# Kernel optimization log

Measured on AMD Instinct MI355X. Metric: run time of the kernel, lower is better.

## Reference

```python
import jax, jax.numpy as jnp
import numpy as np

GN_EPS = 1e-5
G = 8          # SKA groups
SKS3 = 27      # sks**3


def _aff(x, s, b):
    # folded BatchNorm (eval): per-channel scale + shift on NCDHW tensor
    return x * s[None, :, None, None, None] + b[None, :, None, None, None]


def _c1(x, w):
    # 1x1x1 conv as channel GEMM; w: [O, I]
    return jnp.einsum('bcdhw,oc->bodhw', x, w)


def _dw5(x, w):
    # depthwise 5x5x5 conv, pad=2; w: [C, 1, 5, 5, 5]
    return jax.lax.conv_general_dilated(
        x, w, window_strides=(1, 1, 1), padding=[(2, 2)] * 3,
        dimension_numbers=('NCDHW', 'OIDHW', 'NCDHW'),
        feature_group_count=x.shape[1])


def setup_inputs() -> dict:
    key = jax.random.key(0)
    ks = jax.random.split(key, 24)
    B, C, D, H, W = 2, 64, 32, 32, 32

    def n(k, shape, scale=1.0):
        return jax.random.normal(k, shape, jnp.float32) * scale

    def u(k, shape):
        return jax.random.uniform(k, shape, jnp.float32, 0.5, 1.5)

    return {
        'x': n(ks[0], (B, C, D, H, W)),
        'w1': n(ks[1], (32, 64), 64 ** -0.5),
        's1': u(ks[2], (32,)), 'b1': n(ks[3], (32,), 0.1),
        'w2': n(ks[4], (32, 1, 5, 5, 5), 125 ** -0.5),
        's2': u(ks[5], (32,)), 'b2': n(ks[6], (32,), 0.1),
        'w3': n(ks[7], (32, 32), 32 ** -0.5),
        's3': u(ks[8], (32,)), 'b3': n(ks[9], (32,), 0.1),
        'w4': n(ks[10], (216, 32), 32 ** -0.5), 'b4': n(ks[11], (216,), 0.1),
        'gn_g': u(ks[12], (216,)), 'gn_b': n(ks[13], (216,), 0.1),
        'bn_s': u(ks[14], (64,)), 'bn_b': n(ks[15], (64,), 0.1),
        'pw1_w': n(ks[16], (128, 64), 64 ** -0.5),
        'pw1_s': u(ks[17], (128,)), 'pw1_b': n(ks[18], (128,), 0.1),
        'pw2_w': n(ks[19], (64, 128), 128 ** -0.5),
        'pw2_s': u(ks[20], (64,)), 'pw2_b': n(ks[21], (64,), 0.1),
    }


def reference(x, w1, s1, b1, w2, s2, b2, w3, s3, b3, w4, b4,
              gn_g, gn_b, bn_s, bn_b,
              pw1_w, pw1_s, pw1_b, pw2_w, pw2_s, pw2_b):
    B, C, D, H, W = x.shape

    # ---- LKP3D: dynamic kernel generation ----
    a = jax.nn.relu(_aff(_c1(x, w1), s1, b1))          # cv1 + BN + ReLU
    a = _aff(_dw5(a, w2), s2, b2)                      # cv2 (5^3 dw) + BN
    a = jax.nn.relu(_aff(_c1(a, w3), s3, b3))          # cv3 + BN + ReLU
    wk = _c1(a, w4) + b4[None, :, None, None, None]    # cv4: [B,216,D,H,W]
    # GroupNorm: num_groups = dim//groups = 8, channels = 216
    g = wk.reshape(B, G, SKS3, D, H, W)
    mu = g.mean(axis=(2, 3, 4, 5), keepdims=True)
    var = g.var(axis=(2, 3, 4, 5), keepdims=True)
    g = (g - mu) * jax.lax.rsqrt(var + GN_EPS)
    wk = g.reshape(B, G * SKS3, D, H, W) * gn_g[None, :, None, None, None] \
         + gn_b[None, :, None, None, None]
    wk = wk.reshape(B, G, SKS3, D, H, W)               # [B, G, 27, D, H, W]

    # ---- SKA3D: apply dynamic kernels (27 shifted copies, grouped) ----
    offs = [(di, hi, wi) for di in (-1, 0, 1) for hi in (-1, 0, 1) for wi in (-1, 0, 1)]
    patches = jnp.stack(
        [jnp.roll(x, (-di, -hi, -wi), axis=(2, 3, 4)) for di, hi, wi in offs],
        axis=2)                                        # [B, C, 27, D, H, W]
    p = patches.reshape(B, G, C // G, SKS3, D, H, W)
    sk = jnp.einsum('bgckdhw,bgkdhw->bgcdhw', p, wk).reshape(B, C, D, H, W)

    y = _aff(sk, bn_s, bn_b) + x                       # LSConv BN + residual

    # ---- FFN (residual): pw1 + BN + ReLU + pw2 + BN ----
    f = jax.nn.relu(_aff(_c1(y, pw1_w), pw1_s, pw1_b))
    f = _aff(_c1(f, pw2_w), pw2_s, pw2_b)
    return y + f
```

## Files before the change

### kernel.cpp

```cpp
#include <hip/hip_runtime.h>
#include <hip/hip_bf16.h>

#define SPAT 32768
#define BATCH 2
#define GN_EPS 1e-5f

__device__ __forceinline__ void fma4(float4& a, const float4& v, float w) {
    a.x = fmaf(v.x, w, a.x); a.y = fmaf(v.y, w, a.y);
    a.z = fmaf(v.z, w, a.z); a.w = fmaf(v.w, w, a.w);
}

template <bool RELU, bool AFF>
__global__ __launch_bounds__(256) void k_c1(
    const float* __restrict__ in, const float* __restrict__ w,
    const float* __restrict__ sc, const float* __restrict__ bi,
    float* __restrict__ out, int Cin, int Cout)
{
    int q = blockIdx.x * 256 + threadIdx.x;
    int s = q * 4;
    int o0 = blockIdx.y * 4, b = blockIdx.z;
    const float* ip = in + (size_t)b * Cin * SPAT + s;
    float4 a0 = {0,0,0,0}, a1 = a0, a2 = a0, a3 = a0;
#pragma unroll 4
    for (int c = 0; c < Cin; ++c) {
        float4 v = *(const float4*)(ip + (size_t)c * SPAT);
        fma4(a0, v, w[(o0+0)*Cin + c]);
        fma4(a1, v, w[(o0+1)*Cin + c]);
        fma4(a2, v, w[(o0+2)*Cin + c]);
        fma4(a3, v, w[(o0+3)*Cin + c]);
    }
    float4 accs[4] = {a0, a1, a2, a3};
#pragma unroll
    for (int i = 0; i < 4; ++i) {
        int o = o0 + i;
        float scale = AFF ? sc[o] : 1.f;
        float shift = bi[o];
        float4 r = accs[i];
        r.x = r.x * scale + shift; r.y = r.y * scale + shift;
        r.z = r.z * scale + shift; r.w = r.w * scale + shift;
        if (RELU) {
            r.x = fmaxf(r.x, 0.f); r.y = fmaxf(r.y, 0.f);
            r.z = fmaxf(r.z, 0.f); r.w = fmaxf(r.w, 0.f);
        }
        *(float4*)(out + ((size_t)b * Cout + o) * SPAT + s) = r;
    }
}

__global__ __launch_bounds__(256) void k_cv4(
    const float* __restrict__ in, const float* __restrict__ w,
    const float* __restrict__ bi, float* __restrict__ out,
    float* __restrict__ partial)
{
    int q = blockIdx.x * 256 + threadIdx.x;
    int s = q * 4;
    int o0 = blockIdx.y * 4, b = blockIdx.z;
    const float* ip = in + (size_t)b * 32 * SPAT + s;
    float4 a0 = {0,0,0,0}, a1 = a0, a2 = a0, a3 = a0;
#pragma unroll 4
    for (int c = 0; c < 32; ++c) {
        float4 v = *(const float4*)(ip + (size_t)c * SPAT);
        fma4(a0, v, w[(o0+0)*32 + c]);
        fma4(a1, v, w[(o0+1)*32 + c]);
        fma4(a2, v, w[(o0+2)*32 + c]);
        fma4(a3, v, w[(o0+3)*32 + c]);
    }
    float4 accs[4] = {a0, a1, a2, a3};
    float sums[4], sss[4];
#pragma unroll
    for (int i = 0; i < 4; ++i) {
        int o = o0 + i;
        float shift = bi[o];
        float4 r = accs[i];
        r.x += shift; r.y += shift; r.z += shift; r.w += shift;
        *(float4*)(out + ((size_t)b * 216 + o) * SPAT + s) = r;
        sums[i] = r.x + r.y + r.z + r.w;
        sss[i]  = r.x*r.x + r.y*r.y + r.z*r.z + r.w*r.w;
    }
#pragma unroll
    for (int off = 32; off > 0; off >>= 1) {
#pragma unroll
        for (int i = 0; i < 4; ++i) {
            sums[i] += __shfl_down(sums[i], off, 64);
            sss[i]  += __shfl_down(sss[i],  off, 64);
        }
    }
    __shared__ float sh[4][4][2];
    int wave = threadIdx.x >> 6, lane = threadIdx.x & 63;
    if (lane == 0) {
#pragma unroll
        for (int i = 0; i < 4; ++i) {
            sh[wave][i][0] = sums[i];
            sh[wave][i][1] = sss[i];
        }
    }
    __syncthreads();
    if (threadIdx.x < 4) {
        int i = threadIdx.x;
        float s0 = sh[0][i][0] + sh[1][i][0] + sh[2][i][0] + sh[3][i][0];
        float s1 = sh[0][i][1] + sh[1][i][1] + sh[2][i][1] + sh[3][i][1];
        int o = o0 + i;
        int idx = (((b * 216 + o) * 32) + blockIdx.x) * 2;
        partial[idx + 0] = s0;
        partial[idx + 1] = s1;
    }
}

__global__ __launch_bounds__(256) void k_gn_stats2(
    const float* __restrict__ partial, float* __restrict__ stats)
{
    int bg = blockIdx.x;
    int b = bg >> 3, g = bg & 7;
    float sum = 0.f, ss = 0.f;
    for (int i = threadIdx.x; i < 27 * 32; i += 256) {
        int o = g * 27 + (i >> 5);
        int xb = i & 31;
        int idx = ((b * 216 + o) * 32 + xb) * 2;
        sum += partial[idx + 0];
        ss  += partial[idx + 1];
    }
    __shared__ float sh[512];
    sh[threadIdx.x] = sum; sh[256 + threadIdx.x] = ss;
    __syncthreads();
    for (int off = 128; off > 0; off >>= 1) {
        if (threadIdx.x < off) {
            sh[threadIdx.x] += sh[threadIdx.x + off];
            sh[256 + threadIdx.x] += sh[256 + threadIdx.x + off];
        }
        __syncthreads();
    }
    if (threadIdx.x == 0) {
        stats[bg * 2 + 0] = sh[0];
        stats[bg * 2 + 1] = sh[256];
    }
}

__global__ __launch_bounds__(256) void k_ska(
    const float* __restrict__ x, const float* __restrict__ wk,
    const float* __restrict__ stats,
    const float* __restrict__ gn_g, const float* __restrict__ gn_b,
    const float* __restrict__ bn_s, const float* __restrict__ bn_b,
    float* __restrict__ y)
{
    int q = blockIdx.x * 256 + threadIdx.x;
    int s = q * 4;
    int g = blockIdx.y, b = blockIdx.z;
    int bg = b * 8 + g;
    const float N = 27.f * (float)SPAT;
    float mu  = stats[bg * 2 + 0] / N;
    float var = stats[bg * 2 + 1] / N - mu * mu;
    float inv = rsqrtf(var + GN_EPS);
    int d = s >> 10, h = (s >> 5) & 31, w0 = s & 31;
    int lane = threadIdx.x & 63;
    int xl_src = (lane & 56) | ((lane + 7) & 7);
    int xr_src = (lane & 56) | ((lane + 1) & 7);
    const float* xg = x + ((size_t)(b * 64 + g * 8)) * SPAT;
    const float* wp = wk + ((size_t)(b * 216 + g * 27)) * SPAT + s;

    float4 acc[8];
    float4 xc[8];
#pragma unroll
    for (int c = 0; c < 8; ++c) acc[c] = {0,0,0,0};

#pragma unroll
    for (int kd = 0; kd < 3; ++kd) {
        int zd = (d + kd + 31) & 31;
#pragma unroll
        for (int kh = 0; kh < 3; ++kh) {
            int zh = (h + kh + 31) & 31;
            int kbase = (kd * 3 + kh) * 3;
            float wn[3][4];
#pragma unroll
            for (int kw = 0; kw < 3; ++kw) {
                int kk = kbase + kw;
                float4 wq = *(const float4*)(wp + (size_t)kk * SPAT);
                float gg = gn_g[g * 27 + kk], gb = gn_b[g * 27 + kk];
                wn[kw][0] = (wq.x - mu) * inv * gg + gb;
                wn[kw][1] = (wq.y - mu) * inv * gg + gb;
                wn[kw][2] = (wq.z - mu) * inv * gg + gb;
                wn[kw][3] = (wq.w - mu) * inv * gg + gb;
            }
            int rowoff = zd * 1024 + zh * 32;
            bool center = (kd == 1) && (kh == 1);
#pragma unroll
            for (int c = 0; c < 8; ++c) {
                float4 m = *(const float4*)(xg + (size_t)c * SPAT + rowoff + w0);
                if (center) xc[c] = m;
                float xl = __shfl(m.w, xl_src, 64);
                float xr = __shfl(m.x, xr_src, 64);
                float win[6] = {xl, m.x, m.y, m.z, m.w, xr};
#pragma unroll
                for (int kw = 0; kw < 3; ++kw) {
                    acc[c].x = fmaf(win[0 + kw], wn[kw][0], acc[c].x);
                    acc[c].y = fmaf(win[1 + kw], wn[kw][1], acc[c].y);
                    acc[c].z = fmaf(win[2 + kw], wn[kw][2], acc[c].z);
                    acc[c].w = fmaf(win[3 + kw], wn[kw][3], acc[c].w);
                }
            }
        }
    }
#pragma unroll
    for (int c = 0; c < 8; ++c) {
        int ch = g * 8 + c;
        float bs = bn_s[ch], bb = bn_b[ch];
        float4 r;
        r.x = acc[c].x * bs + bb + xc[c].x;
        r.y = acc[c].y * bs + bb + xc[c].y;
        r.z = acc[c].z * bs + bb + xc[c].z;
        r.w = acc[c].w * bs + bb + xc[c].w;
        *(float4*)(y + ((size_t)(b * 64 + ch)) * SPAT + s) = r;
    }
}

__global__ __launch_bounds__(256) void k_dw5(
    const float* __restrict__ in, const float* __restrict__ w2,
    const float* __restrict__ s2, const float* __restrict__ b2,
    float* __restrict__ out)
{
    __shared__ float lds[8 * 36 * 40];
    int tid = threadIdx.x;
    int d0 = blockIdx.x * 4;
    int c = blockIdx.y, b = blockIdx.z;
    const float* ip = in + ((size_t)(b * 32 + c)) * SPAT;

    float4 z = {0,0,0,0};
    for (int i = tid; i < 8 * 36 * 40 / 4; i += 256)
        ((float4*)lds)[i] = z;
    __syncthreads();
    for (int i = tid; i < 8 * 256; i += 256) {
        int p = i >> 8, rem = i & 255;
        int r = rem >> 3, c4 = (rem & 7) * 4;
        int d = d0 - 2 + p;
        if (d >= 0 && d < 32) {
            float4 v = *(const float4*)(ip + d * 1024 + r * 32 + c4);
            *(float4*)&lds[p * 1440 + (r + 2) * 40 + (c4 + 4)] = v;
        }
    }
    __syncthreads();

    float scl = s2[c], shf = b2[c];
    const float* wt = w2 + c * 125;
#pragma unroll
    for (int k = 0; k < 4; ++k) {
        int j = tid + k * 256;
        int pd = j >> 8, rem = j & 255;
        int hr = rem >> 3, w4 = (rem & 7) * 4;
        float4 acc = {0,0,0,0};
#pragma unroll
        for (int kd = 0; kd < 5; ++kd) {
            const float* pl = &lds[(pd + kd) * 1440];
#pragma unroll
            for (int kh = 0; kh < 5; ++kh) {
                const float* row = pl + (hr + kh) * 40 + w4;
                float4 r0 = *(const float4*)(row);
                float4 r1 = *(const float4*)(row + 4);
                float4 r2 = *(const float4*)(row + 8);
                float win[12] = {r0.x, r0.y, r0.z, r0.w,
                                 r1.x, r1.y, r1.z, r1.w,
                                 r2.x, r2.y, r2.z, r2.w};
#pragma unroll
                for (int kw = 0; kw < 5; ++kw) {
                    float wv = wt[kd * 25 + kh * 5 + kw];
                    acc.x = fmaf(wv, win[2 + 0 + kw], acc.x);
                    acc.y = fmaf(wv, win[2 + 1 + kw], acc.y);
                    acc.z = fmaf(wv, win[2 + 2 + kw], acc.z);
                    acc.w = fmaf(wv, win[2 + 3 + kw], acc.w);
                }
            }
        }
        acc.x = acc.x * scl + shf; acc.y = acc.y * scl + shf;
        acc.z = acc.z * scl + shf; acc.w = acc.w * scl + shf;
        *(float4*)(out + ((size_t)(b * 32 + c)) * SPAT
                   + (d0 + pd) * 1024 + hr * 32 + w4) = acc;
    }
}

__global__ __launch_bounds__(256) void k_pw2_out(
    const float* __restrict__ f1, const float* __restrict__ w,
    const float* __restrict__ sc, const float* __restrict__ bi,
    const float* __restrict__ yres, float* __restrict__ out)
{
    int q = blockIdx.x * 256 + threadIdx.x;
    int s = q * 4;
    int o0 = blockIdx.y * 4, b = blockIdx.z;
    const float* ip = f1 + (size_t)b * 128 * SPAT + s;
    float4 a0 = {0,0,0,0}, a1 = a0, a2 = a0, a3 = a0;
#pragma unroll 4
    for (int c = 0; c < 128; ++c) {
        float4 v = *(const float4*)(ip + (size_t)c * SPAT);
        fma4(a0, v, w[(o0+0)*128 + c]);
        fma4(a1, v, w[(o0+1)*128 + c]);
        fma4(a2, v, w[(o0+2)*128 + c]);
        fma4(a3, v, w[(o0+3)*128 + c]);
    }
    float4 accs[4] = {a0, a1, a2, a3};
#pragma unroll
    for (int i = 0; i < 4; ++i) {
        int o = o0 + i;
        float scale = sc[o], shift = bi[o];
        float4 yv = *(const float4*)(yres + ((size_t)(b * 64 + o)) * SPAT + s);
        float4 r = accs[i];
        r.x = r.x * scale + shift + yv.x;
        r.y = r.y * scale + shift + yv.y;
        r.z = r.z * scale + shift + yv.z;
        r.w = r.w * scale + shift + yv.w;
        *(float4*)(out + ((size_t)(b * 64 + o)) * SPAT + s) = r;
    }
}

extern "C" void kernel_launch(void* const* d_in, const int* in_sizes, int n_in,
                              void* d_out, int out_size, void* d_ws, size_t ws_size,
                              hipStream_t stream)
{
    const float* x     = (const float*)d_in[0];
    const float* w1    = (const float*)d_in[1];
    const float* s1    = (const float*)d_in[2];
    const float* b1    = (const float*)d_in[3];
    const float* w2    = (const float*)d_in[4];
    const float* s2    = (const float*)d_in[5];
    const float* b2    = (const float*)d_in[6];
    const float* w3    = (const float*)d_in[7];
    const float* s3    = (const float*)d_in[8];
    const float* b3    = (const float*)d_in[9];
    const float* w4    = (const float*)d_in[10];
    const float* b4    = (const float*)d_in[11];
    const float* gn_g  = (const float*)d_in[12];
    const float* gn_b  = (const float*)d_in[13];
    const float* bn_s  = (const float*)d_in[14];
    const float* bn_b  = (const float*)d_in[15];
    const float* pw1_w = (const float*)d_in[16];
    const float* pw1_s = (const float*)d_in[17];
    const float* pw1_b = (const float*)d_in[18];
    const float* pw2_w = (const float*)d_in[19];
    const float* pw2_s = (const float*)d_in[20];
    const float* pw2_b = (const float*)d_in[21];

    float* ws    = (float*)d_ws;
    float* a1    = ws;
    float* a2    = a1 + (size_t)BATCH * 32 * SPAT;
    float* yb    = ws;
    float* wkb   = ws + (size_t)BATCH * 64 * SPAT;
    float* f1    = wkb;
    float* part  = wkb + (size_t)BATCH * 216 * SPAT;
    float* stats = part + BATCH * 216 * 32 * 2;

    dim3 blk(256);
    k_c1<true, true><<<dim3(SPAT / 1024, 8, BATCH), blk, 0, stream>>>(
        x, w1, s1, b1, a1, 64, 32);
    k_dw5<<<dim3(8, 32, BATCH), blk, 0, stream>>>(a1, w2, s2, b2, a2);
    k_c1<true, true><<<dim3(SPAT / 1024, 8, BATCH), blk, 0, stream>>>(
        a2, w3, s3, b3, a1, 32, 32);
    k_cv4<<<dim3(SPAT / 1024, 54, BATCH), blk, 0, stream>>>(
        a1, w4, b4, wkb, part);
    k_gn_stats2<<<dim3(16, 1, 1), blk, 0, stream>>>(part, stats);
    k_ska<<<dim3(SPAT / 1024, 8, BATCH), blk, 0, stream>>>(
        x, wkb, stats, gn_g, gn_b, bn_s, bn_b, yb);
    k_c1<true, true><<<dim3(SPAT / 1024, 32, BATCH), blk, 0, stream>>>(
        yb, pw1_w, pw1_s, pw1_b, f1, 64, 128);
    k_pw2_out<<<dim3(SPAT / 1024, 16, BATCH), blk, 0, stream>>>(
        f1, pw2_w, pw2_s, pw2_b, yb, (float*)d_out);
}
```

Before: 230.2 us.

## Recompute dynamic kernels inside SKA instead of materializing the 216-channel tensor

The 216-channel cv4 output is no longer written to memory. A stats-only kernel computes the per-group GroupNorm sums with atomics, and the SKA kernel recomputes its group's 27 kernel weights from the 32-channel activation, applying the normalization on the fly. This also removes the separate partial-stats reduction kernel. The pointwise conv kernels now compute more output channels per thread (templated NO) to reuse each input load more. The trade-off is that cv4 arithmetic is done twice and register pressure rises, in exchange for avoiding about 56MB of write plus read traffic.

```diff
diff --git a/kernel.cpp b/kernel.cpp
--- a/kernel.cpp
+++ b/kernel.cpp
@@ -1,5 +1,4 @@
 #include <hip/hip_runtime.h>
-#include <hip/hip_bf16.h>
 
 #define SPAT 32768
 #define BATCH 2
@@ -10,32 +9,36 @@
     a.z = fmaf(v.z, w, a.z); a.w = fmaf(v.w, w, a.w);
 }
 
-template <bool RELU, bool AFF>
+__global__ __launch_bounds__(64) void k_zero(float* __restrict__ p)
+{
+    if (threadIdx.x < 32) p[threadIdx.x] = 0.f;
+}
+
+template <int CIN, int NO, bool RELU>
 __global__ __launch_bounds__(256) void k_c1(
     const float* __restrict__ in, const float* __restrict__ w,
     const float* __restrict__ sc, const float* __restrict__ bi,
-    float* __restrict__ out, int Cin, int Cout)
+    float* __restrict__ out, int Cout)
 {
     int q = blockIdx.x * 256 + threadIdx.x;
     int s = q * 4;
-    int o0 = blockIdx.y * 4, b = blockIdx.z;
-    const float* ip = in + (size_t)b * Cin * SPAT + s;
-    float4 a0 = {0,0,0,0}, a1 = a0, a2 = a0, a3 = a0;
+    int o0 = blockIdx.y * NO, b = blockIdx.z;
+    const float* ip = in + (size_t)b * CIN * SPAT + s;
+    float4 acc[NO];
+#pragma unroll
+    for (int i = 0; i < NO; ++i) acc[i] = {0.f, 0.f, 0.f, 0.f};
 #pragma unroll 4
-    for (int c = 0; c < Cin; ++c) {
+    for (int c = 0; c < CIN; ++c) {
         float4 v = *(const float4*)(ip + (size_t)c * SPAT);
-        fma4(a0, v, w[(o0+0)*Cin + c]);
-        fma4(a1, v, w[(o0+1)*Cin + c]);
-        fma4(a2, v, w[(o0+2)*Cin + c]);
-        fma4(a3, v, w[(o0+3)*Cin + c]);
-    }
-    float4 accs[4] = {a0, a1, a2, a3};
-#pragma unroll
-    for (int i = 0; i < 4; ++i) {
+#pragma unroll
+        for (int i = 0; i < NO; ++i)
+            fma4(acc[i], v, w[(o0 + i) * CIN + c]);
+    }
+#pragma unroll
+    for (int i = 0; i < NO; ++i) {
         int o = o0 + i;
-        float scale = AFF ? sc[o] : 1.f;
-        float shift = bi[o];
-        float4 r = accs[i];
+        float scale = sc[o], shift = bi[o];
+        float4 r = acc[i];
         r.x = r.x * scale + shift; r.y = r.y * scale + shift;
         r.z = r.z * scale + shift; r.w = r.w * scale + shift;
         if (RELU) {
@@ -46,96 +49,54 @@
     }
 }
 
-__global__ __launch_bounds__(256) void k_cv4(
-    const float* __restrict__ in, const float* __restrict__ w,
-    const float* __restrict__ bi, float* __restrict__ out,
-    float* __restrict__ partial)
+__global__ __launch_bounds__(256) void k_cv4_stats(
+    const float* __restrict__ a, const float* __restrict__ w4,
+    const float* __restrict__ b4, float* __restrict__ stats)
 {
     int q = blockIdx.x * 256 + threadIdx.x;
     int s = q * 4;
-    int o0 = blockIdx.y * 4, b = blockIdx.z;
-    const float* ip = in + (size_t)b * 32 * SPAT + s;
-    float4 a0 = {0,0,0,0}, a1 = a0, a2 = a0, a3 = a0;
-#pragma unroll 4
+    int g = blockIdx.y, b = blockIdx.z;
+    const float* ip = a + (size_t)b * 32 * SPAT + s;
+    const float* wg = w4 + g * 27 * 32;
+    float4 wk[27];
+#pragma unroll
+    for (int k = 0; k < 27; ++k) {
+        float bv = b4[g * 27 + k];
+        wk[k] = {bv, bv, bv, bv};
+    }
+#pragma unroll 2
     for (int c = 0; c < 32; ++c) {
         float4 v = *(const float4*)(ip + (size_t)c * SPAT);
-        fma4(a0, v, w[(o0+0)*32 + c]);
-        fma4(a1, v, w[(o0+1)*32 + c]);
-        fma4(a2, v, w[(o0+2)*32 + c]);
-        fma4(a3, v, w[(o0+3)*32 + c]);
-    }
-    float4 accs[4] = {a0, a1, a2, a3};
-    float sums[4], sss[4];
-#pragma unroll
-    for (int i = 0; i < 4; ++i) {
-        int o = o0 + i;
-        float shift = bi[o];
-        float4 r = accs[i];
-        r.x += shift; r.y += shift; r.z += shift; r.w += shift;
-        *(float4*)(out + ((size_t)b * 216 + o) * SPAT + s) = r;
-        sums[i] = r.x + r.y + r.z + r.w;
-        sss[i]  = r.x*r.x + r.y*r.y + r.z*r.z + r.w*r.w;
+#pragma unroll
+        for (int k = 0; k < 27; ++k)
+            fma4(wk[k], v, wg[k * 32 + c]);
+    }
+    float sum = 0.f, ss = 0.f;
+#pragma unroll
+    for (int k = 0; k < 27; ++k) {
+        sum += wk[k].x + wk[k].y + wk[k].z + wk[k].w;
+        ss  += wk[k].x * wk[k].x + wk[k].y * wk[k].y
+             + wk[k].z * wk[k].z + wk[k].w * wk[k].w;
     }
 #pragma unroll
     for (int off = 32; off > 0; off >>= 1) {
-#pragma unroll
-        for (int i = 0; i < 4; ++i) {
-            sums[i] += __shfl_down(sums[i], off, 64);
-            sss[i]  += __shfl_down(sss[i],  off, 64);
-        }
-    }
-    __shared__ float sh[4][4][2];
+        sum += __shfl_down(sum, off, 64);
+        ss  += __shfl_down(ss,  off, 64);
+    }
+    __shared__ float sh[8];
     int wave = threadIdx.x >> 6, lane = threadIdx.x & 63;
-    if (lane == 0) {
-#pragma unroll
-        for (int i = 0; i < 4; ++i) {
-            sh[wave][i][0] = sums[i];
-            sh[wave][i][1] = sss[i];
-        }
-    }
+    if (lane == 0) { sh[wave * 2] = sum; sh[wave * 2 + 1] = ss; }
     __syncthreads();
-    if (threadIdx.x < 4) {
-        int i = threadIdx.x;
-        float s0 = sh[0][i][0] + sh[1][i][0] + sh[2][i][0] + sh[3][i][0];
-        float s1 = sh[0][i][1] + sh[1][i][1] + sh[2][i][1] + sh[3][i][1];
-        int o = o0 + i;
-        int idx = (((b * 216 + o) * 32) + blockIdx.x) * 2;
-        partial[idx + 0] = s0;
-        partial[idx + 1] = s1;
-    }
-}
-
-__global__ __launch_bounds__(256) void k_gn_stats2(
-    const float* __restrict__ partial, float* __restrict__ stats)
-{
-    int bg = blockIdx.x;
-    int b = bg >> 3, g = bg & 7;
-    float sum = 0.f, ss = 0.f;
-    for (int i = threadIdx.x; i < 27 * 32; i += 256) {
-        int o = g * 27 + (i >> 5);
-        int xb = i & 31;
-        int idx = ((b * 216 + o) * 32 + xb) * 2;
-        sum += partial[idx + 0];
-        ss  += partial[idx + 1];
-    }
-    __shared__ float sh[512];
-    sh[threadIdx.x] = sum; sh[256 + threadIdx.x] = ss;
-    __syncthreads();
-    for (int off = 128; off > 0; off >>= 1) {
-        if (threadIdx.x < off) {
-            sh[threadIdx.x] += sh[threadIdx.x + off];
-            sh[256 + threadIdx.x] += sh[256 + threadIdx.x + off];
-        }
-        __syncthreads();
-    }
     if (threadIdx.x == 0) {
-        stats[bg * 2 + 0] = sh[0];
-        stats[bg * 2 + 1] = sh[256];
+        int bg = b * 8 + g;
+        atomicAdd(&stats[bg * 2 + 0], sh[0] + sh[2] + sh[4] + sh[6]);
+        atomicAdd(&stats[bg * 2 + 1], sh[1] + sh[3] + sh[5] + sh[7]);
     }
 }
 
 __global__ __launch_bounds__(256) void k_ska(
-    const float* __restrict__ x, const float* __restrict__ wk,
+    const float* __restrict__ x, const float* __restrict__ a1,
+    const float* __restrict__ w4, const float* __restrict__ b4,
     const float* __restrict__ stats,
     const float* __restrict__ gn_g, const float* __restrict__ gn_b,
     const float* __restrict__ bn_s, const float* __restrict__ bn_b,
@@ -154,31 +115,43 @@
     int xl_src = (lane & 56) | ((lane + 7) & 7);
     int xr_src = (lane & 56) | ((lane + 1) & 7);
     const float* xg = x + ((size_t)(b * 64 + g * 8)) * SPAT;
-    const float* wp = wk + ((size_t)(b * 216 + g * 27)) * SPAT + s;
+    const float* ag = a1 + (size_t)b * 32 * SPAT + s;
+    const float* wg = w4 + g * 27 * 32;
 
     float4 acc[8];
     float4 xc[8];
 #pragma unroll
-    for (int c = 0; c < 8; ++c) acc[c] = {0,0,0,0};
+    for (int c = 0; c < 8; ++c) acc[c] = {0.f, 0.f, 0.f, 0.f};
 
 #pragma unroll
     for (int kd = 0; kd < 3; ++kd) {
+        float4 wk9[9];
+#pragma unroll
+        for (int j = 0; j < 9; ++j) {
+            float bv = b4[g * 27 + kd * 9 + j];
+            wk9[j] = {bv, bv, bv, bv};
+        }
+#pragma unroll 4
+        for (int c = 0; c < 32; ++c) {
+            float4 v = *(const float4*)(ag + (size_t)c * SPAT);
+#pragma unroll
+            for (int j = 0; j < 9; ++j)
+                fma4(wk9[j], v, wg[(kd * 9 + j) * 32 + c]);
+        }
+#pragma unroll
+        for (int j = 0; j < 9; ++j) {
+            int kk = kd * 9 + j;
+            float gg = gn_g[g * 27 + kk] * inv;
+            float sgb = gn_b[g * 27 + kk] - mu * gg;
+            wk9[j].x = wk9[j].x * gg + sgb;
+            wk9[j].y = wk9[j].y * gg + sgb;
+            wk9[j].z = wk9[j].z * gg + sgb;
+            wk9[j].w = wk9[j].w * gg + sgb;
+        }
         int zd = (d + kd + 31) & 31;
 #pragma unroll
         for (int kh = 0; kh < 3; ++kh) {
             int zh = (h + kh + 31) & 31;
-            int kbase = (kd * 3 + kh) * 3;
-            float wn[3][4];
-#pragma unroll
-            for (int kw = 0; kw < 3; ++kw) {
-                int kk = kbase + kw;
-                float4 wq = *(const float4*)(wp + (size_t)kk * SPAT);
-                float gg = gn_g[g * 27 + kk], gb = gn_b[g * 27 + kk];
-                wn[kw][0] = (wq.x - mu) * inv * gg + gb;
-                wn[kw][1] = (wq.y - mu) * inv * gg + gb;
-                wn[kw][2] = (wq.z - mu) * inv * gg + gb;
-                wn[kw][3] = (wq.w - mu) * inv * gg + gb;
-            }
             int rowoff = zd * 1024 + zh * 32;
             bool center = (kd == 1) && (kh == 1);
 #pragma unroll
@@ -190,10 +163,11 @@
                 float win[6] = {xl, m.x, m.y, m.z, m.w, xr};
 #pragma unroll
                 for (int kw = 0; kw < 3; ++kw) {
-                    acc[c].x = fmaf(win[0 + kw], wn[kw][0], acc[c].x);
-                    acc[c].y = fmaf(win[1 + kw], wn[kw][1], acc[c].y);
-                    acc[c].z = fmaf(win[2 + kw], wn[kw][2], acc[c].z);
-                    acc[c].w = fmaf(win[3 + kw], wn[kw][3], acc[c].w);
+                    float4 wn = wk9[kh * 3 + kw];
+                    acc[c].x = fmaf(win[0 + kw], wn.x, acc[c].x);
+                    acc[c].y = fmaf(win[1 + kw], wn.y, acc[c].y);
+                    acc[c].z = fmaf(win[2 + kw], wn.z, acc[c].z);
+                    acc[c].w = fmaf(win[3 + kw], wn.w, acc[c].w);
                 }
             }
         }
@@ -222,7 +196,7 @@
     int c = blockIdx.y, b = blockIdx.z;
     const float* ip = in + ((size_t)(b * 32 + c)) * SPAT;
 
-    float4 z = {0,0,0,0};
+    float4 z = {0.f, 0.f, 0.f, 0.f};
     for (int i = tid; i < 8 * 36 * 40 / 4; i += 256)
         ((float4*)lds)[i] = z;
     __syncthreads();
@@ -243,14 +217,14 @@
     for (int k = 0; k < 4; ++k) {
         int j = tid + k * 256;
         int pd = j >> 8, rem = j & 255;
-        int hr = rem >> 3, w4 = (rem & 7) * 4;
-        float4 acc = {0,0,0,0};
+        int hr = rem >> 3, w4i = (rem & 7) * 4;
+        float4 acc = {0.f, 0.f, 0.f, 0.f};
 #pragma unroll
         for (int kd = 0; kd < 5; ++kd) {
             const float* pl = &lds[(pd + kd) * 1440];
 #pragma unroll
             for (int kh = 0; kh < 5; ++kh) {
-                const float* row = pl + (hr + kh) * 40 + w4;
+                const float* row = pl + (hr + kh) * 40 + w4i;
                 float4 r0 = *(const float4*)(row);
                 float4 r1 = *(const float4*)(row + 4);
                 float4 r2 = *(const float4*)(row + 8);
@@ -270,10 +244,11 @@
         acc.x = acc.x * scl + shf; acc.y = acc.y * scl + shf;
         acc.z = acc.z * scl + shf; acc.w = acc.w * scl + shf;
         *(float4*)(out + ((size_t)(b * 32 + c)) * SPAT
-                   + (d0 + pd) * 1024 + hr * 32 + w4) = acc;
-    }
-}
-
+                   + (d0 + pd) * 1024 + hr * 32 + w4i) = acc;
+    }
+}
+
+template <int NO>
 __global__ __launch_bounds__(256) void k_pw2_out(
     const float* __restrict__ f1, const float* __restrict__ w,
     const float* __restrict__ sc, const float* __restrict__ bi,
@@ -281,24 +256,24 @@
 {
     int q = blockIdx.x * 256 + threadIdx.x;
     int s = q * 4;
-    int o0 = blockIdx.y * 4, b = blockIdx.z;
+    int o0 = blockIdx.y * NO, b = blockIdx.z;
     const float* ip = f1 + (size_t)b * 128 * SPAT + s;
-    float4 a0 = {0,0,0,0}, a1 = a0, a2 = a0, a3 = a0;
+    float4 acc[NO];
+#pragma unroll
+    for (int i = 0; i < NO; ++i) acc[i] = {0.f, 0.f, 0.f, 0.f};
 #pragma unroll 4
     for (int c = 0; c < 128; ++c) {
         float4 v = *(const float4*)(ip + (size_t)c * SPAT);
-        fma4(a0, v, w[(o0+0)*128 + c]);
-        fma4(a1, v, w[(o0+1)*128 + c]);
-        fma4(a2, v, w[(o0+2)*128 + c]);
-        fma4(a3, v, w[(o0+3)*128 + c]);
-    }
-    float4 accs[4] = {a0, a1, a2, a3};
-#pragma unroll
-    for (int i = 0; i < 4; ++i) {
+#pragma unroll
+        for (int i = 0; i < NO; ++i)
+            fma4(acc[i], v, w[(o0 + i) * 128 + c]);
+    }
+#pragma unroll
+    for (int i = 0; i < NO; ++i) {
         int o = o0 + i;
         float scale = sc[o], shift = bi[o];
         float4 yv = *(const float4*)(yres + ((size_t)(b * 64 + o)) * SPAT + s);
-        float4 r = accs[i];
+        float4 r = acc[i];
         r.x = r.x * scale + shift + yv.x;
         r.y = r.y * scale + shift + yv.y;
         r.z = r.z * scale + shift + yv.z;
@@ -337,25 +312,23 @@
     float* ws    = (float*)d_ws;
     float* a1    = ws;
     float* a2    = a1 + (size_t)BATCH * 32 * SPAT;
-    float* yb    = ws;
-    float* wkb   = ws + (size_t)BATCH * 64 * SPAT;
-    float* f1    = wkb;
-    float* part  = wkb + (size_t)BATCH * 216 * SPAT;
-    float* stats = part + BATCH * 216 * 32 * 2;
+    float* yb    = a2 + (size_t)BATCH * 32 * SPAT;
+    float* f1    = yb + (size_t)BATCH * 64 * SPAT;
+    float* stats = f1 + (size_t)BATCH * 128 * SPAT;
 
     dim3 blk(256);
-    k_c1<true, true><<<dim3(SPAT / 1024, 8, BATCH), blk, 0, stream>>>(
-        x, w1, s1, b1, a1, 64, 32);
+    k_zero<<<dim3(1), dim3(64), 0, stream>>>(stats);
+    k_c1<64, 8, true><<<dim3(SPAT / 1024, 4, BATCH), blk, 0, stream>>>(
+        x, w1, s1, b1, a1, 32);
     k_dw5<<<dim3(8, 32, BATCH), blk, 0, stream>>>(a1, w2, s2, b2, a2);
-    k_c1<true, true><<<dim3(SPAT / 1024, 8, BATCH), blk, 0, stream>>>(
-        a2, w3, s3, b3, a1, 32, 32);
-    k_cv4<<<dim3(SPAT / 1024, 54, BATCH), blk, 0, stream>>>(
-        a1, w4, b4, wkb, part);
-    k_gn_stats2<<<dim3(16, 1, 1), blk, 0, stream>>>(part, stats);
+    k_c1<32, 8, true><<<dim3(SPAT / 1024, 4, BATCH), blk, 0, stream>>>(
+        a2, w3, s3, b3, a1, 32);
+    k_cv4_stats<<<dim3(SPAT / 1024, 8, BATCH), blk, 0, stream>>>(
+        a1, w4, b4, stats);
     k_ska<<<dim3(SPAT / 1024, 8, BATCH), blk, 0, stream>>>(
-        x, wkb, stats, gn_g, gn_b, bn_s, bn_b, yb);
-    k_c1<true, true><<<dim3(SPAT / 1024, 32, BATCH), blk, 0, stream>>>(
-        yb, pw1_w, pw1_s, pw1_b, f1, 64, 128);
-    k_pw2_out<<<dim3(SPAT / 1024, 16, BATCH), blk, 0, stream>>>(
+        x, a1, w4, b4, stats, gn_g, gn_b, bn_s, bn_b, yb);
+    k_c1<64, 16, true><<<dim3(SPAT / 1024, 8, BATCH), blk, 0, stream>>>(
+        yb, pw1_w, pw1_s, pw1_b, f1, 128);
+    k_pw2_out<16><<<dim3(SPAT / 1024, 4, BATCH), blk, 0, stream>>>(
         f1, pw2_w, pw2_s, pw2_b, yb, (float*)d_out);
 }
```

Result: slower. 266.2 us (+15.6%).

## Fuse FFN pw1 and pw2 into one per-voxel register-resident kernel

Applied to the files above, without the earlier changes.

Replaces the two FFN kernels (pw1 writing a 128-channel intermediate to global memory, then pw2 reading it back) with a single kernel. Each thread holds one voxel's 64 input channels and 64 output accumulators in registers and processes the hidden channels in chunks of 16. This removes the global write and read of the large hidden tensor and one launch. In exchange it needs heavy register use, so occupancy drops to about one block per CU, with only 256 blocks in the grid, and weights are read as uniform scalar loads per thread.

```diff
diff --git a/kernel.cpp b/kernel.cpp
--- a/kernel.cpp
+++ b/kernel.cpp
@@ -1,5 +1,4 @@
 #include <hip/hip_runtime.h>
-#include <hip/hip_bf16.h>
 
 #define SPAT 32768
 #define BATCH 2
@@ -243,14 +242,14 @@
     for (int k = 0; k < 4; ++k) {
         int j = tid + k * 256;
         int pd = j >> 8, rem = j & 255;
-        int hr = rem >> 3, w4 = (rem & 7) * 4;
+        int hr = rem >> 3, w4i = (rem & 7) * 4;
         float4 acc = {0,0,0,0};
 #pragma unroll
         for (int kd = 0; kd < 5; ++kd) {
             const float* pl = &lds[(pd + kd) * 1440];
 #pragma unroll
             for (int kh = 0; kh < 5; ++kh) {
-                const float* row = pl + (hr + kh) * 40 + w4;
+                const float* row = pl + (hr + kh) * 40 + w4i;
                 float4 r0 = *(const float4*)(row);
                 float4 r1 = *(const float4*)(row + 4);
                 float4 r2 = *(const float4*)(row + 8);
@@ -270,41 +269,52 @@
         acc.x = acc.x * scl + shf; acc.y = acc.y * scl + shf;
         acc.z = acc.z * scl + shf; acc.w = acc.w * scl + shf;
         *(float4*)(out + ((size_t)(b * 32 + c)) * SPAT
-                   + (d0 + pd) * 1024 + hr * 32 + w4) = acc;
-    }
-}
-
-__global__ __launch_bounds__(256) void k_pw2_out(
-    const float* __restrict__ f1, const float* __restrict__ w,
-    const float* __restrict__ sc, const float* __restrict__ bi,
-    const float* __restrict__ yres, float* __restrict__ out)
-{
-    int q = blockIdx.x * 256 + threadIdx.x;
-    int s = q * 4;
-    int o0 = blockIdx.y * 4, b = blockIdx.z;
-    const float* ip = f1 + (size_t)b * 128 * SPAT + s;
-    float4 a0 = {0,0,0,0}, a1 = a0, a2 = a0, a3 = a0;
-#pragma unroll 4
-    for (int c = 0; c < 128; ++c) {
-        float4 v = *(const float4*)(ip + (size_t)c * SPAT);
-        fma4(a0, v, w[(o0+0)*128 + c]);
-        fma4(a1, v, w[(o0+1)*128 + c]);
-        fma4(a2, v, w[(o0+2)*128 + c]);
-        fma4(a3, v, w[(o0+3)*128 + c]);
-    }
-    float4 accs[4] = {a0, a1, a2, a3};
-#pragma unroll
-    for (int i = 0; i < 4; ++i) {
-        int o = o0 + i;
-        float scale = sc[o], shift = bi[o];
-        float4 yv = *(const float4*)(yres + ((size_t)(b * 64 + o)) * SPAT + s);
-        float4 r = accs[i];
-        r.x = r.x * scale + shift + yv.x;
-        r.y = r.y * scale + shift + yv.y;
-        r.z = r.z * scale + shift + yv.z;
-        r.w = r.w * scale + shift + yv.w;
-        *(float4*)(out + ((size_t)(b * 64 + o)) * SPAT + s) = r;
-    }
+                   + (d0 + pd) * 1024 + hr * 32 + w4i) = acc;
+    }
+}
+
+__global__ __launch_bounds__(256, 1) void k_ffn(
+    const float* __restrict__ yin,
+    const float* __restrict__ w1v, const float* __restrict__ s1v,
+    const float* __restrict__ b1v,
+    const float* __restrict__ w2v, const float* __restrict__ s2v,
+    const float* __restrict__ b2v,
+    float* __restrict__ out)
+{
+    int pos = blockIdx.x * 256 + threadIdx.x;
+    int b = blockIdx.z;
+    const float* ip = yin + (size_t)b * 64 * SPAT + pos;
+    float y[64];
+#pragma unroll
+    for (int c = 0; c < 64; ++c) y[c] = ip[(size_t)c * SPAT];
+    float acc[64];
+#pragma unroll
+    for (int o = 0; o < 64; ++o) acc[o] = 0.f;
+#pragma unroll 1
+    for (int fc0 = 0; fc0 < 128; fc0 += 16) {
+        float f[16];
+#pragma unroll
+        for (int j = 0; j < 16; ++j) {
+            float a = 0.f;
+#pragma unroll
+            for (int c = 0; c < 64; ++c)
+                a = fmaf(y[c], w1v[(fc0 + j) * 64 + c], a);
+            a = a * s1v[fc0 + j] + b1v[fc0 + j];
+            f[j] = fmaxf(a, 0.f);
+        }
+#pragma unroll
+        for (int o = 0; o < 64; ++o) {
+            float a = acc[o];
+#pragma unroll
+            for (int j = 0; j < 16; ++j)
+                a = fmaf(f[j], w2v[o * 128 + fc0 + j], a);
+            acc[o] = a;
+        }
+    }
+    float* op = out + (size_t)b * 64 * SPAT + pos;
+#pragma unroll
+    for (int o = 0; o < 64; ++o)
+        op[(size_t)o * SPAT] = acc[o] * s2v[o] + b2v[o] + y[o];
 }
 
 extern "C" void kernel_launch(void* const* d_in, const int* in_sizes, int n_in,
@@ -339,7 +349,6 @@
     float* a2    = a1 + (size_t)BATCH * 32 * SPAT;
     float* yb    = ws;
     float* wkb   = ws + (size_t)BATCH * 64 * SPAT;
-    float* f1    = wkb;
     float* part  = wkb + (size_t)BATCH * 216 * SPAT;
     float* stats = part + BATCH * 216 * 32 * 2;
 
@@ -354,8 +363,6 @@
     k_gn_stats2<<<dim3(16, 1, 1), blk, 0, stream>>>(part, stats);
     k_ska<<<dim3(SPAT / 1024, 8, BATCH), blk, 0, stream>>>(
         x, wkb, stats, gn_g, gn_b, bn_s, bn_b, yb);
-    k_c1<true, true><<<dim3(SPAT / 1024, 32, BATCH), blk, 0, stream>>>(
-        yb, pw1_w, pw1_s, pw1_b, f1, 64, 128);
-    k_pw2_out<<<dim3(SPAT / 1024, 16, BATCH), blk, 0, stream>>>(
-        f1, pw2_w, pw2_s, pw2_b, yb, (float*)d_out);
-}
+    k_ffn<<<dim3(SPAT / 256, 1, BATCH), blk, 0, stream>>>(
+        yb, pw1_w, pw1_s, pw1_b, pw2_w, pw2_s, pw2_b, (float*)d_out);
+}
```

Result: slower. 437.5 us (+90.0%).
